# Performance work log

Hardware: AMD Instinct MI355X
Metric: run time of the kernel (lower is better)

Reference implementation:

```python
import jax, jax.numpy as jnp
import numpy as np
from jax import lax

CENSUS_R = 3
EDGE_WEIGHT = 4.0


def _grayscale(img):
    # ITU-R 601 luma, as in tf.image.rgb_to_grayscale used by UnFlow-style census
    w = jnp.array([0.299, 0.587, 0.114], dtype=img.dtype)
    return jnp.einsum('bchw,c->bhw', img, w)[:, None]  # (B,1,H,W)


def _grid(H, W, dtype):
    gy, gx = jnp.meshgrid(jnp.arange(H, dtype=dtype), jnp.arange(W, dtype=dtype), indexing='ij')
    return gy, gx


def _warp_bilinear(img, flow):
    # Resample2d: out(x,y) = img(x + u, y + v), bilinear, clamped at borders.
    B, C, H, W = img.shape
    gy, gx = _grid(H, W, flow.dtype)
    x = gx[None] + flow[:, 0]   # (B,H,W)
    y = gy[None] + flow[:, 1]
    x0 = jnp.floor(x); y0 = jnp.floor(y)
    wx = (x - x0)[:, None]; wy = (y - y0)[:, None]  # (B,1,H,W)
    x0i = jnp.clip(x0.astype(jnp.int32), 0, W - 1)
    x1i = jnp.clip(x0i + 1, 0, W - 1)
    y0i = jnp.clip(y0.astype(jnp.int32), 0, H - 1)
    y1i = jnp.clip(y0i + 1, 0, H - 1)
    flat = img.reshape(B, C, H * W)

    def gather(yi, xi):
        idx = (yi * W + xi).reshape(B, 1, H * W)
        return jnp.take_along_axis(flat, idx, axis=2).reshape(B, C, H, W)

    return (gather(y0i, x0i) * (1.0 - wx) * (1.0 - wy)
            + gather(y0i, x1i) * wx * (1.0 - wy)
            + gather(y1i, x0i) * (1.0 - wx) * wy
            + gather(y1i, x1i) * wx * wy)


def _border_mask(flow):
    # 1 where the flow target lands inside the image, 0 otherwise. (B,1,H,W)
    B, _, H, W = flow.shape
    gy, gx = _grid(H, W, flow.dtype)
    x = gx[None] + flow[:, 0]
    y = gy[None] + flow[:, 1]
    inside = (x >= 0) & (x <= W - 1) & (y >= 0) & (y <= H - 1)
    return inside[:, None].astype(flow.dtype)


def _charbonnier(x, mask=None, alpha=0.45, eps=1e-3):
    err = (x * x + eps * eps) ** alpha
    if mask is not None:
        err = err * mask
    return jnp.sum(err) / x.size


def _census_transform(img, r):
    gray = _grayscale(img) * 255.0
    p = 2 * r + 1
    # identity kernel extracts the (2r+1)^2 neighborhood per pixel
    k = jnp.asarray(np.eye(p * p, dtype=np.float32).reshape(p * p, 1, p, p))
    patches = lax.conv_general_dilated(gray, k, (1, 1), 'SAME',
                                       dimension_numbers=('NCHW', 'OIHW', 'NCHW'))
    d = patches - gray  # (B,p*p,H,W)
    return d / jnp.sqrt(0.81 + d * d)


def _census_loss(img1, img2_warp, mask, r):
    t1 = _census_transform(img1, r)
    t2 = _census_transform(img2_warp, r)
    dist = (t1 - t2) ** 2
    dist = dist / (0.1 + dist)                 # soft hamming per neighbor
    dist = jnp.sum(dist, axis=1, keepdims=True)  # (B,1,H,W)
    B, _, H, W = img1.shape
    inner = jnp.zeros((1, 1, H, W), img1.dtype).at[:, :, r:H - r, r:W - r].set(1.0)
    return _charbonnier(dist, mask * inner)


def _smooth_grad_1st(flow, img, edge_weight):
    img_dx = img[:, :, :, :-1] - img[:, :, :, 1:]
    img_dy = img[:, :, :-1, :] - img[:, :, 1:, :]
    w_x = jnp.exp(-jnp.mean(jnp.abs(img_dx), axis=1, keepdims=True) * edge_weight)
    w_y = jnp.exp(-jnp.mean(jnp.abs(img_dy), axis=1, keepdims=True) * edge_weight)
    f_dx = flow[:, :, :, :-1] - flow[:, :, :, 1:]
    f_dy = flow[:, :, :-1, :] - flow[:, :, 1:, :]
    pen = lambda d: (d * d + 1e-6) ** 0.45  # charbonnier penalty
    return 0.5 * (jnp.mean(w_x * pen(f_dx)) + jnp.mean(w_y * pen(f_dy)))


def setup_inputs() -> dict:
    key = jax.random.key(0)
    k1, k2, k3, k4 = jax.random.split(key, 4)
    B, H, W = 8, 448, 1024
    return {
        'flow1': jax.random.normal(k1, (B, 2, H, W), dtype=jnp.float32),
        'target1': jax.random.normal(k2, (B, 2, H, W), dtype=jnp.float32),
        'input1': jax.random.uniform(k3, (B, 3, H, W), dtype=jnp.float32),
        'input2': jax.random.uniform(k4, (B, 3, H, W), dtype=jnp.float32),
    }


def reference(flow1, target1, input1, input2):
    mask = _border_mask(flow1)
    img2_warp = _warp_bilinear(input2, flow1)
    census = 1.0 * _census_loss(input1, img2_warp, mask, CENSUS_R)
    smooth = 1.0 * _smooth_grad_1st(flow1, input1, EDGE_WEIGHT)
    energy = census + smooth
    epe = jnp.mean(jnp.sqrt(jnp.sum((flow1 - target1) ** 2, axis=1)))
    return (energy, epe)
```

## Files before the change

kernel.cpp:

```cpp
#include <hip/hip_runtime.h>
#include <math.h>

#define BB 8
#define HH 448
#define WW 1024
#define HWSZ (HH*WW)
#define NPIX (BB*HH*WW)
#define CR 3
#define TX 64
#define TY 16
#define HX (TX+2*CR)
#define HY (TY+2*CR)
#define NB1 (HH*BB)
#define NB2 (16*28*BB)

__device__ __forceinline__ float pen45(float dd) {
    return __expf(0.45f * __logf(dd));
}


__global__ __launch_bounds__(256) void k_prep(
    const float* __restrict__ flow, const float* __restrict__ target,
    const float* __restrict__ img1, const float* __restrict__ img2,
    float* __restrict__ g1, float* __restrict__ g2,
    float* __restrict__ part_sx, float* __restrict__ part_sy, float* __restrict__ part_epe)
{
    const int tid = threadIdx.x;
    const int y = blockIdx.x;
    const int b = blockIdx.y;
    const int x = tid * 4;
    const int idx = y * WW + x;
    const float* i1r = img1 + (size_t)b * 3 * HWSZ;
    const float* i1g = i1r + HWSZ;
    const float* i1b = i1r + 2 * HWSZ;
    const float* i2r = img2 + (size_t)b * 3 * HWSZ;
    const float* i2g = i2r + HWSZ;
    const float* i2b = i2r + 2 * HWSZ;
    const float* fu = flow + (size_t)b * 2 * HWSZ;
    const float* fv = fu + HWSZ;
    const float* tu = target + (size_t)b * 2 * HWSZ;
    const float* tv = tu + HWSZ;

    float4 a1r = *(const float4*)(i1r + idx);
    float4 a1g = *(const float4*)(i1g + idx);
    float4 a1b = *(const float4*)(i1b + idx);
    float4 a2r = *(const float4*)(i2r + idx);
    float4 a2g = *(const float4*)(i2g + idx);
    float4 a2b = *(const float4*)(i2b + idx);
    float4 au  = *(const float4*)(fu + idx);
    float4 av  = *(const float4*)(fv + idx);
    float4 atu = *(const float4*)(tu + idx);
    float4 atv = *(const float4*)(tv + idx);

    const int nf = (tid == 255) ? 3 : 4;
    float nr = i1r[idx + nf], ng = i1g[idx + nf], nb = i1b[idx + nf];
    float nu = fu[idx + nf],  nv = fv[idx + nf];

    float4 l1, l2;
    l1.x = (0.299f*a1r.x + 0.587f*a1g.x + 0.114f*a1b.x) * 255.0f;
    l1.y = (0.299f*a1r.y + 0.587f*a1g.y + 0.114f*a1b.y) * 255.0f;
    l1.z = (0.299f*a1r.z + 0.587f*a1g.z + 0.114f*a1b.z) * 255.0f;
    l1.w = (0.299f*a1r.w + 0.587f*a1g.w + 0.114f*a1b.w) * 255.0f;
    l2.x = (0.299f*a2r.x + 0.587f*a2g.x + 0.114f*a2b.x) * 255.0f;
    l2.y = (0.299f*a2r.y + 0.587f*a2g.y + 0.114f*a2b.y) * 255.0f;
    l2.z = (0.299f*a2r.z + 0.587f*a2g.z + 0.114f*a2b.z) * 255.0f;
    l2.w = (0.299f*a2r.w + 0.587f*a2g.w + 0.114f*a2b.w) * 255.0f;
    *(float4*)(g1 + (size_t)b * HWSZ + idx) = l1;
    *(float4*)(g2 + (size_t)b * HWSZ + idx) = l2;

    float A1r[5] = {a1r.x, a1r.y, a1r.z, a1r.w, nr};
    float A1g[5] = {a1g.x, a1g.y, a1g.z, a1g.w, ng};
    float A1b[5] = {a1b.x, a1b.y, a1b.z, a1b.w, nb};
    float FU[5]  = {au.x, au.y, au.z, au.w, nu};
    float FV[5]  = {av.x, av.y, av.z, av.w, nv};
    float TU[4]  = {atu.x, atu.y, atu.z, atu.w};
    float TV[4]  = {atv.x, atv.y, atv.z, atv.w};

    float ep = 0.0f, sx = 0.0f, sy = 0.0f;
    #pragma unroll
    for (int k = 0; k < 4; k++) {
        float du = FU[k] - TU[k], dv = FV[k] - TV[k];
        ep += sqrtf(du * du + dv * dv);
        float ad = fabsf(A1r[k] - A1r[k+1]) + fabsf(A1g[k] - A1g[k+1]) + fabsf(A1b[k] - A1b[k+1]);
        float wx = __expf(-(4.0f / 3.0f) * ad);
        float d0 = FU[k] - FU[k+1], d1 = FV[k] - FV[k+1];
        float t = wx * (pen45(fmaf(d0, d0, 1e-6f)) + pen45(fmaf(d1, d1, 1e-6f)));
        if (x + k < WW - 1) sx += t;
    }

    if (y < HH - 1) {
        float4 b1r = *(const float4*)(i1r + idx + WW);
        float4 b1g = *(const float4*)(i1g + idx + WW);
        float4 b1b = *(const float4*)(i1b + idx + WW);
        float4 bu  = *(const float4*)(fu + idx + WW);
        float4 bv  = *(const float4*)(fv + idx + WW);
        float B1r[4] = {b1r.x, b1r.y, b1r.z, b1r.w};
        float B1g[4] = {b1g.x, b1g.y, b1g.z, b1g.w};
        float B1b[4] = {b1b.x, b1b.y, b1b.z, b1b.w};
        float BU[4]  = {bu.x, bu.y, bu.z, bu.w};
        float BV[4]  = {bv.x, bv.y, bv.z, bv.w};
        #pragma unroll
        for (int k = 0; k < 4; k++) {
            float ad = fabsf(A1r[k] - B1r[k]) + fabsf(A1g[k] - B1g[k]) + fabsf(A1b[k] - B1b[k]);
            float wy = __expf(-(4.0f / 3.0f) * ad);
            float d0 = FU[k] - BU[k], d1 = FV[k] - BV[k];
            sy += wy * (pen45(fmaf(d0, d0, 1e-6f)) + pen45(fmaf(d1, d1, 1e-6f)));
        }
    }

    #pragma unroll
    for (int off = 32; off; off >>= 1) {
        ep += __shfl_down(ep, off);
        sx += __shfl_down(sx, off);
        sy += __shfl_down(sy, off);
    }
    __shared__ float red[3][4];
    const int lane = tid & 63, wid = tid >> 6;
    if (lane == 0) { red[0][wid] = sx; red[1][wid] = sy; red[2][wid] = ep; }
    __syncthreads();
    if (tid == 0) {
        const int bid = b * HH + y;
        part_sx[bid]  = red[0][0] + red[0][1] + red[0][2] + red[0][3];
        part_sy[bid]  = red[1][0] + red[1][1] + red[1][2] + red[1][3];
        part_epe[bid] = red[2][0] + red[2][1] + red[2][2] + red[2][3];
    }
}

__global__ __launch_bounds__(256) void k_census(
    const float* __restrict__ flow,
    const float* __restrict__ g1, const float* __restrict__ g2,
    float* __restrict__ part_cen)
{
    __shared__ float t1s[HY][HX];
    __shared__ float t2s[HY][HX];
    __shared__ unsigned char mks[HY][HX];

    const int b = blockIdx.z;
    const int x0 = CR + blockIdx.x * TX;
    const int y0 = CR + blockIdx.y * TY;
    const float* g1b = g1 + (size_t)b * HWSZ;
    const float* g2b = g2 + (size_t)b * HWSZ;
    const float* fl = flow + (size_t)b * 2 * HWSZ;
    const int tid = threadIdx.x;

    for (int i = tid; i < HY * HX; i += 256) {
        int ly = i / HX, lx = i - ly * HX;
        int gx = x0 - CR + lx; if (gx > WW - 1) gx = WW - 1;
        int gy = y0 - CR + ly; if (gy > HH - 1) gy = HH - 1;
        int gidx = gy * WW + gx;
        t1s[ly][lx] = g1b[gidx];
        float u = fl[gidx], v = fl[HWSZ + gidx];
        float xx = (float)gx + u, yy = (float)gy + v;
        float fx = floorf(xx), fy = floorf(yy);
        float wx = xx - fx, wy = yy - fy;
        int xi0 = (int)fx; xi0 = xi0 < 0 ? 0 : (xi0 > WW - 1 ? WW - 1 : xi0);
        int xi1 = xi0 + 1 > WW - 1 ? WW - 1 : xi0 + 1;
        int yi0 = (int)fy; yi0 = yi0 < 0 ? 0 : (yi0 > HH - 1 ? HH - 1 : yi0);
        int yi1 = yi0 + 1 > HH - 1 ? HH - 1 : yi0 + 1;
        float v00 = g2b[yi0 * WW + xi0], v01 = g2b[yi0 * WW + xi1];
        float v10 = g2b[yi1 * WW + xi0], v11 = g2b[yi1 * WW + xi1];
        t2s[ly][lx] = v00 * ((1.0f - wx) * (1.0f - wy)) + v01 * (wx * (1.0f - wy))
                    + v10 * ((1.0f - wx) * wy) + v11 * (wx * wy);
        mks[ly][lx] = (unsigned char)((xx >= 0.0f) && (xx <= (float)(WW - 1)) &&
                                      (yy >= 0.0f) && (yy <= (float)(HH - 1)));
    }
    __syncthreads();

    const int lx = tid & 63;
    const int lyb = tid >> 6;
    float sum = 0.0f;
    #pragma unroll
    for (int j = 0; j < 4; j++) {
        const int ly = j * 4 + lyb;
        const int cx = x0 + lx, cy = y0 + ly;
        const bool valid = (cx <= WW - 1 - CR) && (cy <= HH - 1 - CR);
        const int hx = lx + CR, hy = ly + CR;
        const float c1 = t1s[hy][hx];
        const float c2 = t2s[hy][hx];
        float dist = 0.0f;
        #pragma unroll
        for (int dy = -CR; dy <= CR; dy++) {
            #pragma unroll
            for (int dx = -CR; dx <= CR; dx++) {
                if (dx == 0 && dy == 0) continue;
                float d1 = t1s[hy + dy][hx + dx] - c1;
                float d2 = t2s[hy + dy][hx + dx] - c2;
                float t1 = d1 * __builtin_amdgcn_rsqf(fmaf(d1, d1, 0.81f));
                float t2 = d2 * __builtin_amdgcn_rsqf(fmaf(d2, d2, 0.81f));
                float dd = t1 - t2;
                float s = dd * dd;
                dist = fmaf(s, __builtin_amdgcn_rcpf(0.1f + s), dist);
            }
        }
        if (valid && mks[hy][hx]) {
            sum += pen45(fmaf(dist, dist, 1e-6f));
        }
    }

    #pragma unroll
    for (int off = 32; off; off >>= 1) sum += __shfl_down(sum, off);
    __shared__ float rs[4];
    if ((tid & 63) == 0) rs[tid >> 6] = sum;
    __syncthreads();
    if (tid == 0) {
        const int bid = (b * gridDim.y + blockIdx.y) * gridDim.x + blockIdx.x;
        part_cen[bid] = rs[0] + rs[1] + rs[2] + rs[3];
    }
}

__global__ __launch_bounds__(256) void k_final(
    const float* __restrict__ part_sx, const float* __restrict__ part_sy,
    const float* __restrict__ part_epe, const float* __restrict__ part_cen,
    float* __restrict__ out)
{
    const int tid = threadIdx.x;
    float sx = 0.f, sy = 0.f, ep = 0.f, cn = 0.f;
    for (int i = tid; i < NB1; i += 256) {
        sx += part_sx[i]; sy += part_sy[i]; ep += part_epe[i];
    }
    for (int i = tid; i < NB2; i += 256) cn += part_cen[i];
    #pragma unroll
    for (int off = 32; off; off >>= 1) {
        sx += __shfl_down(sx, off); sy += __shfl_down(sy, off);
        ep += __shfl_down(ep, off); cn += __shfl_down(cn, off);
    }
    __shared__ float r[4][4];
    const int lane = tid & 63, wid = tid >> 6;
    if (lane == 0) { r[0][wid] = sx; r[1][wid] = sy; r[2][wid] = ep; r[3][wid] = cn; }
    __syncthreads();
    if (tid == 0) {
        sx = r[0][0] + r[0][1] + r[0][2] + r[0][3];
        sy = r[1][0] + r[1][1] + r[1][2] + r[1][3];
        ep = r[2][0] + r[2][1] + r[2][2] + r[2][3];
        cn = r[3][0] + r[3][1] + r[3][2] + r[3][3];
        float census = cn / (float)NPIX;
        float mx = sx / (float)((size_t)BB * 2 * HH * (WW - 1));
        float my = sy / (float)((size_t)BB * 2 * (HH - 1) * WW);
        out[0] = census + 0.5f * (mx + my);
        out[1] = ep / (float)NPIX;
    }
}

extern "C" void kernel_launch(void* const* d_in, const int* in_sizes, int n_in,
                              void* d_out, int out_size, void* d_ws, size_t ws_size,
                              hipStream_t stream) {
    const float* flow   = (const float*)d_in[0];
    const float* target = (const float*)d_in[1];
    const float* img1   = (const float*)d_in[2];
    const float* img2   = (const float*)d_in[3];
    float* out = (float*)d_out;

    float* part_sx  = (float*)d_ws;
    float* part_sy  = part_sx + NB1;
    float* part_epe = part_sy + NB1;
    float* part_cen = part_epe + NB1;
    float* g1 = (float*)((char*)d_ws + 65536);
    float* g2 = g1 + (size_t)NPIX;

    dim3 gr1(HH, BB, 1);
    k_prep<<<gr1, dim3(256, 1, 1), 0, stream>>>(flow, target, img1, img2, g1, g2,
                                                part_sx, part_sy, part_epe);

    dim3 gr2((WW - 2 * CR + TX - 1) / TX, (HH - 2 * CR + TY - 1) / TY, BB);
    k_census<<<gr2, dim3(256, 1, 1), 0, stream>>>(flow, g1, g2, part_cen);

    k_final<<<1, dim3(256, 1, 1), 0, stream>>>(part_sx, part_sy, part_epe, part_cen, out);
}
```

Baseline: 258.0 us.

## Register-block census: four pixels per thread with float4 row loads from padded LDS

The census kernel now gives each thread four horizontally adjacent pixels and loads each of the seven stencil rows once as twelve values via float4 reads from a padded shared tile (row pitch 72). This replaces 48 scalar LDS reads per pixel with shared row vectors reused across the four outputs, cutting LDS traffic and address arithmetic. The mask becomes a float array covering only the interior, read with one float4. The cost is higher register pressure and a different thread-to-pixel mapping. The transcendental work per pixel is unchanged, so the kernel may already be limited by ALU throughput.

```diff
diff --git a/kernel.cpp b/kernel.cpp
--- a/kernel.cpp
+++ b/kernel.cpp
@@ -10,6 +10,7 @@
 #define TX 64
 #define TY 16
 #define HX (TX+2*CR)
+#define HXP 72
 #define HY (TY+2*CR)
 #define NB1 (HH*BB)
 #define NB2 (16*28*BB)
@@ -131,9 +132,9 @@
     const float* __restrict__ g1, const float* __restrict__ g2,
     float* __restrict__ part_cen)
 {
-    __shared__ float t1s[HY][HX];
-    __shared__ float t2s[HY][HX];
-    __shared__ unsigned char mks[HY][HX];
+    __shared__ float t1s[HY][HXP];
+    __shared__ float t2s[HY][HXP];
+    __shared__ float mks[TY][TX];
 
     const int b = blockIdx.z;
     const int x0 = CR + blockIdx.x * TX;
@@ -161,40 +162,85 @@
         float v10 = g2b[yi1 * WW + xi0], v11 = g2b[yi1 * WW + xi1];
         t2s[ly][lx] = v00 * ((1.0f - wx) * (1.0f - wy)) + v01 * (wx * (1.0f - wy))
                     + v10 * ((1.0f - wx) * wy) + v11 * (wx * wy);
-        mks[ly][lx] = (unsigned char)((xx >= 0.0f) && (xx <= (float)(WW - 1)) &&
-                                      (yy >= 0.0f) && (yy <= (float)(HH - 1)));
+        if (lx >= CR && lx < CR + TX && ly >= CR && ly < CR + TY)
+            mks[ly - CR][lx - CR] = (float)((xx >= 0.0f) && (xx <= (float)(WW - 1)) &&
+                                            (yy >= 0.0f) && (yy <= (float)(HH - 1)));
     }
     __syncthreads();
 
-    const int lx = tid & 63;
-    const int lyb = tid >> 6;
-    float sum = 0.0f;
-    #pragma unroll
-    for (int j = 0; j < 4; j++) {
-        const int ly = j * 4 + lyb;
-        const int cx = x0 + lx, cy = y0 + ly;
-        const bool valid = (cx <= WW - 1 - CR) && (cy <= HH - 1 - CR);
-        const int hx = lx + CR, hy = ly + CR;
-        const float c1 = t1s[hy][hx];
-        const float c2 = t2s[hy][hx];
-        float dist = 0.0f;
+    const int txg = tid & 15;
+    const int ty  = tid >> 4;
+    const int lxb = txg * 4;
+    const int rowc = ty + CR;
+
+    float dist[4] = {0.f, 0.f, 0.f, 0.f};
+    float c1[4], c2[4];
+
+#define LOADROW(ROW, V1, V2)                                            \
+    float V1[12], V2[12];                                               \
+    {                                                                   \
+        float4 _a0 = *(const float4*)&t1s[ROW][lxb];                    \
+        float4 _a1 = *(const float4*)&t1s[ROW][lxb + 4];                \
+        float4 _a2 = *(const float4*)&t1s[ROW][lxb + 8];                \
+        float4 _b0 = *(const float4*)&t2s[ROW][lxb];                    \
+        float4 _b1 = *(const float4*)&t2s[ROW][lxb + 4];                \
+        float4 _b2 = *(const float4*)&t2s[ROW][lxb + 8];                \
+        V1[0]=_a0.x; V1[1]=_a0.y; V1[2]=_a0.z; V1[3]=_a0.w;             \
+        V1[4]=_a1.x; V1[5]=_a1.y; V1[6]=_a1.z; V1[7]=_a1.w;             \
+        V1[8]=_a2.x; V1[9]=_a2.y; V1[10]=_a2.z; V1[11]=_a2.w;           \
+        V2[0]=_b0.x; V2[1]=_b0.y; V2[2]=_b0.z; V2[3]=_b0.w;             \
+        V2[4]=_b1.x; V2[5]=_b1.y; V2[6]=_b1.z; V2[7]=_b1.w;             \
+        V2[8]=_b2.x; V2[9]=_b2.y; V2[10]=_b2.z; V2[11]=_b2.w;           \
+    }
+
+#define PAIR(V1, V2, K, DX)                                              \
+    {                                                                    \
+        float _d1 = V1[3 + (K) + (DX)] - c1[K];                          \
+        float _d2 = V2[3 + (K) + (DX)] - c2[K];                          \
+        float _u1 = _d1 * __builtin_amdgcn_rsqf(fmaf(_d1, _d1, 0.81f));  \
+        float _u2 = _d2 * __builtin_amdgcn_rsqf(fmaf(_d2, _d2, 0.81f));  \
+        float _dd = _u1 - _u2;                                           \
+        float _s = _dd * _dd;                                            \
+        dist[K] = fmaf(_s, __builtin_amdgcn_rcpf(0.1f + _s), dist[K]);   \
+    }
+
+    {
+        LOADROW(rowc, v1, v2)
         #pragma unroll
-        for (int dy = -CR; dy <= CR; dy++) {
+        for (int k = 0; k < 4; k++) { c1[k] = v1[3 + k]; c2[k] = v2[3 + k]; }
+        #pragma unroll
+        for (int k = 0; k < 4; k++) {
             #pragma unroll
             for (int dx = -CR; dx <= CR; dx++) {
-                if (dx == 0 && dy == 0) continue;
-                float d1 = t1s[hy + dy][hx + dx] - c1;
-                float d2 = t2s[hy + dy][hx + dx] - c2;
-                float t1 = d1 * __builtin_amdgcn_rsqf(fmaf(d1, d1, 0.81f));
-                float t2 = d2 * __builtin_amdgcn_rsqf(fmaf(d2, d2, 0.81f));
-                float dd = t1 - t2;
-                float s = dd * dd;
-                dist = fmaf(s, __builtin_amdgcn_rcpf(0.1f + s), dist);
+                if (dx == 0) continue;
+                PAIR(v1, v2, k, dx)
             }
         }
-        if (valid && mks[hy][hx]) {
-            sum += pen45(fmaf(dist, dist, 1e-6f));
+    }
+    #pragma unroll
+    for (int dyi = 0; dyi < 6; dyi++) {
+        const int dy = (dyi < 3) ? (dyi - 3) : (dyi - 2);
+        const int row = rowc + dy;
+        LOADROW(row, v1, v2)
+        #pragma unroll
+        for (int k = 0; k < 4; k++) {
+            #pragma unroll
+            for (int dx = -CR; dx <= CR; dx++) {
+                PAIR(v1, v2, k, dx)
+            }
         }
+    }
+
+    float sum = 0.0f;
+    const int cy = y0 + ty;
+    const float4 mk = *(const float4*)&mks[ty][lxb];
+    const float mka[4] = {mk.x, mk.y, mk.z, mk.w};
+    #pragma unroll
+    for (int k = 0; k < 4; k++) {
+        const int cx = x0 + lxb + k;
+        const bool valid = (cx <= WW - 1 - CR) && (cy <= HH - 1 - CR);
+        float m = valid ? mka[k] : 0.0f;
+        sum += m * pen45(fmaf(dist[k], dist[k], 1e-6f));
     }
 
     #pragma unroll
@@ -206,6 +252,8 @@
         const int bid = (b * gridDim.y + blockIdx.y) * gridDim.x + blockIdx.x;
         part_cen[bid] = rs[0] + rs[1] + rs[2] + rs[3];
     }
+#undef LOADROW
+#undef PAIR
 }
 
 __global__ __launch_bounds__(256) void k_final(
```

Measured after the change: 254.2 us. Within noise of the previous version (-1.5%).
